# Kernel tuning notes

Hardware: AMD Instinct MI355X
Metric: run time of the kernel (lower is better)

## Reference

```python
import jax, jax.numpy as jnp
import numpy as np
import math

B, T, C = 2, 2048, 2048
NH = 16
HS = C // NH            # 128
N_ELEM = int(0.5 * HS)  # 64, rotary_percentage=0.5
A_T = 10                # adapter_prompt_length


def setup_inputs() -> dict:
    key = jax.random.key(0)
    ks = jax.random.split(key, 8)
    x = jax.random.normal(ks[0], (B, T, C), dtype=jnp.float32)
    # RoPE cache: standard cos/sin of shape (T, n_elem)
    theta = 10000.0 ** (-jnp.arange(0, N_ELEM, 2, dtype=jnp.float32) / N_ELEM)
    pos = jnp.arange(T, dtype=jnp.float32)
    ang = pos[:, None] * theta[None, :]           # (T, n_elem/2)
    ang = jnp.concatenate([ang, ang], axis=-1)    # (T, n_elem)
    cos, sin = jnp.cos(ang), jnp.sin(ang)
    mask = jnp.tril(jnp.ones((T, T), dtype=bool))  # causal
    s = 0.02
    attn_w = jax.random.normal(ks[1], (3 * C, C), dtype=jnp.float32) * s
    attn_b = jax.random.normal(ks[2], (3 * C,), dtype=jnp.float32) * s
    proj_w = jax.random.normal(ks[3], (C, C), dtype=jnp.float32) * s
    proj_b = jax.random.normal(ks[4], (C,), dtype=jnp.float32) * s
    adapter_wte = jax.random.normal(ks[5], (A_T, C), dtype=jnp.float32) * s
    gating_factor = jnp.full((1,), 0.1, dtype=jnp.float32)  # nonzero so adapter path matters
    return {"x": x, "cos": cos, "sin": sin, "mask": mask,
            "attn_w": attn_w, "attn_b": attn_b, "proj_w": proj_w, "proj_b": proj_b,
            "adapter_wte": adapter_wte, "gating_factor": gating_factor}


def apply_rope(t, cos, sin):
    # t: (B, nh, T, n_elem); cos/sin: (T, n_elem)
    half = t.shape[-1] // 2
    t1, t2 = t[..., :half], t[..., half:]
    rotated = jnp.concatenate([-t2, t1], axis=-1)
    return t * cos + rotated * sin


def sdpa(q, k, v, mask, scale):
    # q: (B,nh,Tq,hs), k/v: (B,nh,Tk,hs); mask: bool broadcastable to (Tq,Tk) or None
    s = jnp.einsum('bhqd,bhkd->bhqk', q, k) * scale
    if mask is not None:
        s = jnp.where(mask, s, jnp.finfo(s.dtype).min)
    p = jax.nn.softmax(s, axis=-1)
    return jnp.einsum('bhqk,bhkd->bhqd', p, v)


def reference(x, cos, sin, mask, attn_w, attn_b, proj_w, proj_b, adapter_wte, gating_factor):
    scale = 1.0 / math.sqrt(HS)
    qkv = x @ attn_w.T + attn_b                    # (B,T,3C)
    qkv = qkv.reshape(B, T, NH, 3 * HS).transpose(0, 2, 1, 3)  # (B,nh,T,3hs)
    q, k, v = jnp.split(qkv, 3, axis=-1)           # each (B,nh,T,hs)
    q = jnp.concatenate([apply_rope(q[..., :N_ELEM], cos, sin), q[..., N_ELEM:]], axis=-1)
    k = jnp.concatenate([apply_rope(k[..., :N_ELEM], cos, sin), k[..., N_ELEM:]], axis=-1)
    y = sdpa(q, k, v, mask, scale)                 # (B,nh,T,hs)
    # adapter-prefix attention
    a_qkv = adapter_wte @ attn_w.T + attn_b        # (aT, 3C)
    _, ak, av = jnp.split(a_qkv, 3, axis=-1)       # (aT, C) each
    ak = ak.reshape(1, A_T, NH, HS).transpose(0, 2, 1, 3)  # (1,nh,aT,hs)
    av = av.reshape(1, A_T, NH, HS).transpose(0, 2, 1, 3)
    ak = jnp.broadcast_to(ak, (B, NH, A_T, HS))
    av = jnp.broadcast_to(av, (B, NH, A_T, HS))
    ay = sdpa(q, ak, av, None, scale)              # full (no mask)
    y = y + gating_factor * ay
    y = y.transpose(0, 2, 1, 3).reshape(B, T, C)
    return y @ proj_w.T + proj_b
```

## Files before the change

### kernel.cpp

```cpp
#include <hip/hip_runtime.h>
#include <math.h>

#define B_DIM 2
#define T_DIM 2048
#define C_DIM 2048
#define NHEAD 16
#define HS 128
#define QKV_N 6144
#define AT 10
#define M_DIM 4096

using bf16x8 = __attribute__((ext_vector_type(8))) short;
using f32x4v = __attribute__((ext_vector_type(4))) float;

__device__ __forceinline__ unsigned short f2bf(float f) {
    union { float f; unsigned int u; } cv; cv.f = f;
    unsigned int u = cv.u;
    return (unsigned short)((u + 0x7FFFu + ((u >> 16) & 1u)) >> 16);
}
__device__ __forceinline__ float bf2f(unsigned short h) {
    union { unsigned int u; float f; } cv; cv.u = ((unsigned int)h) << 16;
    return cv.f;
}
__device__ __forceinline__ unsigned int pack_bf16(float lo, float hi) {
    unsigned int r;
    asm volatile("v_cvt_pk_bf16_f32 %0, %1, %2" : "=v"(r) : "v"(lo), "v"(hi));
    return r;
}
__device__ __forceinline__ void gload_lds16(const void* g, void* l) {
    __builtin_amdgcn_global_load_lds(
        (const __attribute__((address_space(1))) void*)g,
        (__attribute__((address_space(3))) void*)l, 16, 0, 0);
}

__global__ __launch_bounds__(256)
void f32_to_bf16_kernel(const float* __restrict__ in, unsigned short* __restrict__ out, int n8) {
    const int i = blockIdx.x * 256 + threadIdx.x;
    if (i >= n8) return;
    const float4 a = *(const float4*)&in[(size_t)i * 8];
    const float4 b = *(const float4*)&in[(size_t)i * 8 + 4];
    *(ushort4*)&out[(size_t)i * 8]     = make_ushort4(f2bf(a.x), f2bf(a.y), f2bf(a.z), f2bf(a.w));
    *(ushort4*)&out[(size_t)i * 8 + 4] = make_ushort4(f2bf(b.x), f2bf(b.y), f2bf(b.z), f2bf(b.w));
}

template<int FUSED>
__global__ __launch_bounds__(256)
void gemm_pipe(const unsigned short* __restrict__ A, const unsigned short* __restrict__ Bw,
               const float* __restrict__ bias, float* __restrict__ Cf32,
               const float* __restrict__ cosb, const float* __restrict__ sinb,
               unsigned short* __restrict__ Qb, unsigned short* __restrict__ Kb,
               unsigned short* __restrict__ Vt, int M, int N, int K) {
    __shared__ unsigned short As[3][4096];
    __shared__ unsigned short Bs[3][4096];

    const int tid  = threadIdx.x;
    const int wave = tid >> 6;
    const int lane = tid & 63;

    const int ncnt = gridDim.x, mcnt = gridDim.y;
    const int nwg = ncnt * mcnt;
    int bid = blockIdx.y * ncnt + blockIdx.x;
    bid = (bid & 7) * (nwg >> 3) + (bid >> 3);
    const int mt = (bid >> 3) % mcnt;
    const int nt = (bid / (mcnt * 8)) * 8 + (bid & 7);
    const int m0 = mt * 128, n0 = nt * 128;

    const int wr = (wave >> 1) * 64;
    const int wc = (wave & 1) * 64;
    const int fr = lane & 15;
    const int hi = lane >> 4;

    const int srow = lane >> 2;
    const int sk   = 8 * ((lane & 3) ^ ((lane >> 3) & 3));
    const int swk  = 8 * (hi ^ ((fr >> 1) & 3));

    auto STAGE = [&](int ks, int bi) {
        const int k0 = ks << 5;
#pragma unroll
        for (int t = 0; t < 2; ++t) {
            const int seg = wave * 2 + t;
            gload_lds16(&A[(size_t)(m0 + seg * 16 + srow) * K + k0 + sk], &As[bi][seg * 512]);
            gload_lds16(&Bw[(size_t)(n0 + seg * 16 + srow) * K + k0 + sk], &Bs[bi][seg * 512]);
        }
    };

    f32x4v acc[4][4];
#pragma unroll
    for (int i = 0; i < 4; ++i)
#pragma unroll
        for (int j = 0; j < 4; ++j)
#pragma unroll
            for (int q = 0; q < 4; ++q) acc[i][j][q] = 0.f;

    const int nk = K >> 5;
    STAGE(0, 0);
    STAGE(1, 1);

    for (int ks = 0; ks < nk; ++ks) {
        if (ks < nk - 1) asm volatile("s_waitcnt vmcnt(4)" ::: "memory");
        else             asm volatile("s_waitcnt vmcnt(0)" ::: "memory");
        __builtin_amdgcn_sched_barrier(0);
        __builtin_amdgcn_s_barrier();
        asm volatile("" ::: "memory");
        __builtin_amdgcn_sched_barrier(0);

        const unsigned short* Ab = As[ks % 3];
        const unsigned short* Bb = Bs[ks % 3];
        bf16x8 af[4], bfg[4];
#pragma unroll
        for (int i = 0; i < 4; ++i)
            af[i] = *(const bf16x8*)&Ab[(wr + i * 16 + fr) * 32 + swk];
#pragma unroll
        for (int j = 0; j < 4; ++j)
            bfg[j] = *(const bf16x8*)&Bb[(wc + j * 16 + fr) * 32 + swk];

        if (ks + 2 < nk) STAGE(ks + 2, (ks + 2) % 3);

        __builtin_amdgcn_s_setprio(1);
#pragma unroll
        for (int i = 0; i < 4; ++i)
#pragma unroll
            for (int j = 0; j < 4; ++j)
                acc[i][j] = __builtin_amdgcn_mfma_f32_16x16x32_bf16(af[i], bfg[j], acc[i][j], 0, 0, 0);
        __builtin_amdgcn_s_setprio(0);
    }

    const int r4 = hi * 4;
    if constexpr (FUSED) {
        const int part = (n0 >> 7) % 3;
        const int head = n0 / 384;
        const int bh   = (m0 >> 11) * NHEAD + head;
        if (part == 2) {
#pragma unroll
            for (int i = 0; i < 4; ++i) {
                const int t0v = (m0 & (T_DIM - 1)) + wr + i * 16 + r4;
#pragma unroll
                for (int j = 0; j < 4; ++j) {
                    const int d = wc + j * 16 + fr;
                    const float bv = bias[n0 + d];
                    ushort4 o = make_ushort4(f2bf(acc[i][j][0] + bv), f2bf(acc[i][j][1] + bv),
                                             f2bf(acc[i][j][2] + bv), f2bf(acc[i][j][3] + bv));
                    *(ushort4*)&Vt[((size_t)bh * HS + d) * T_DIM + t0v] = o;
                }
            }
        } else {
            unsigned short* Dst = part ? Kb : Qb;
            if (wc == 0) {
#pragma unroll
                for (int i = 0; i < 4; ++i) {
#pragma unroll
                    for (int q = 0; q < 4; ++q) {
                        const int t = (m0 & (T_DIM - 1)) + wr + i * 16 + r4 + q;
                        const float* crow = &cosb[t * 64];
                        const float* srw  = &sinb[t * 64];
                        unsigned short* drow = &Dst[((size_t)bh * T_DIM + t) * HS];
#pragma unroll
                        for (int j = 0; j < 2; ++j) {
                            const int d = j * 16 + fr;
                            const float v1 = acc[i][j][q]     + bias[n0 + d];
                            const float v2 = acc[i][j + 2][q] + bias[n0 + d + 32];
                            drow[d]      = f2bf(v1 * crow[d]      - v2 * srw[d]);
                            drow[d + 32] = f2bf(v2 * crow[d + 32] + v1 * srw[d + 32]);
                        }
                    }
                }
            } else {
#pragma unroll
                for (int i = 0; i < 4; ++i) {
                    const int t0r = (m0 & (T_DIM - 1)) + wr + i * 16 + r4;
#pragma unroll
                    for (int j = 0; j < 4; ++j) {
                        const int d = 64 + j * 16 + fr;
                        const float bv = bias[n0 + d];
                        unsigned short* dcol = &Dst[((size_t)bh * T_DIM + t0r) * HS + d];
#pragma unroll
                        for (int q = 0; q < 4; ++q)
                            dcol[(size_t)q * HS] = f2bf(acc[i][j][q] + bv);
                    }
                }
            }
        }
    } else {
#pragma unroll
        for (int i = 0; i < 4; ++i) {
#pragma unroll
            for (int j = 0; j < 4; ++j) {
                const int col = n0 + wc + j * 16 + fr;
                const float bv = bias[col];
#pragma unroll
                for (int q = 0; q < 4; ++q) {
                    const int row = m0 + wr + i * 16 + r4 + q;
                    Cf32[(size_t)row * N + col] = acc[i][j][q] + bv;
                }
            }
        }
    }
}

__global__ __launch_bounds__(64)
void adapter_qkv_kernel(const float* __restrict__ wte, const unsigned short* __restrict__ wb,
                        const float* __restrict__ bias, float* __restrict__ aqkv) {
    const int n = blockIdx.x;
    const int lane = threadIdx.x;
    float acc[AT];
#pragma unroll
    for (int a = 0; a < AT; ++a) acc[a] = 0.f;
    for (int k = lane * 8; k < C_DIM; k += 64 * 8) {
        const ushort4 wa = *(const ushort4*)&wb[(size_t)n * C_DIM + k];
        const ushort4 wc = *(const ushort4*)&wb[(size_t)n * C_DIM + k + 4];
        const float w0 = bf2f(wa.x), w1 = bf2f(wa.y), w2 = bf2f(wa.z), w3 = bf2f(wa.w);
        const float w4 = bf2f(wc.x), w5 = bf2f(wc.y), w6 = bf2f(wc.z), w7 = bf2f(wc.w);
#pragma unroll
        for (int a = 0; a < AT; ++a) {
            const float4 t0 = *(const float4*)&wte[(size_t)a * C_DIM + k];
            const float4 t1 = *(const float4*)&wte[(size_t)a * C_DIM + k + 4];
            acc[a] += w0 * t0.x + w1 * t0.y + w2 * t0.z + w3 * t0.w
                    + w4 * t1.x + w5 * t1.y + w6 * t1.z + w7 * t1.w;
        }
    }
#pragma unroll
    for (int a = 0; a < AT; ++a) {
        float v = acc[a];
        for (int off = 32; off; off >>= 1) v += __shfl_down(v, off);
        if (lane == 0) aqkv[(size_t)a * QKV_N + n] = v + bias[n];
    }
}

__global__ __launch_bounds__(256)
void flash_mfma(const unsigned short* __restrict__ Qb, const unsigned short* __restrict__ Kb,
                const unsigned short* __restrict__ Vt, const float* __restrict__ aqkv,
                const float* __restrict__ gating, unsigned short* __restrict__ yb) {
    __shared__ __align__(16) unsigned short smem[2][16384];

    const int tid = threadIdx.x;
    const int wave = tid >> 6, lane = tid & 63;
    const int lo = lane & 15, hi = lane >> 4;

    const int z = blockIdx.x & 15;
    const int h = (blockIdx.x >> 4) & 15;
    const int b = blockIdx.x >> 8;
    const int bh = b * NHEAD + h;
    const float kscale = 0.08838834764831845f * 1.4426950408889634f;

    const unsigned short* Qh = Qb + (size_t)bh * T_DIM * HS;
    const unsigned short* Kh = Kb + (size_t)bh * T_DIM * HS;
    const unsigned short* Vh = Vt + (size_t)bh * HS * T_DIM;

    float* AK = (float*)&smem[0][0];
    float* AV = AK + AT * HS;

    auto STAGE = [&](int k0, int bufi) {
        unsigned short* Kd = &smem[bufi][0];
        unsigned short* Vd = &smem[bufi][8192];
#pragma unroll
        for (int t = 0; t < 4; ++t) {
            const int kr = wave * 16 + t * 4 + hi;
            gload_lds16(Kh + (size_t)(k0 + kr) * HS + 8 * (lo ^ (kr & 7)),
                        &Kd[(wave * 16 + t * 4) * 128]);
            const int vr = (wave * 4 + t) * 8 + (lane >> 3);
            gload_lds16(Vh + (size_t)vr * T_DIM + k0 + 8 * ((lane & 7) ^ (vr & 7)),
                        &Vd[(wave * 4 + t) * 8 * 64]);
        }
    };

#pragma unroll 1
    for (int pass = 0; pass < 2; ++pass) {
        const int qt = pass ? z : (31 - z);
        const int q0 = qt * 64;
        const int myqrow = q0 + wave * 16 + lo;

        bf16x8 qf[4];
        {
            const unsigned short* qrow = Qh + (size_t)myqrow * HS;
#pragma unroll
            for (int c = 0; c < 4; ++c) qf[c] = *(const bf16x8*)&qrow[c * 32 + hi * 8];
        }

        f32x4v oacc[8];
#pragma unroll
        for (int d = 0; d < 8; ++d)
#pragma unroll
            for (int q = 0; q < 4; ++q) oacc[d][q] = 0.f;
        float m = -INFINITY, ln = 0.f;

        STAGE(0, 0);
        int cur = 0;
        for (int kt = 0; kt <= qt; ++kt) {
            const int k0 = kt * 64;
            __syncthreads();
            if (kt < qt) STAGE(k0 + 64, cur ^ 1);
            const unsigned short* Ks = &smem[cur][0];
            const unsigned short* Vs = &smem[cur][8192];

            f32x4v sacc[4];
            __builtin_amdgcn_s_setprio(1);
#pragma unroll
            for (int s = 0; s < 4; ++s) {
#pragma unroll
                for (int q = 0; q < 4; ++q) sacc[s][q] = 0.f;
                const int krow = s * 16 + lo;
                const int rs = (lo & 7) << 4;
#pragma unroll
                for (int c = 0; c < 4; ++c) {
                    const int boff = (c * 64 + hi * 16) ^ rs;
                    bf16x8 kf = *(const bf16x8*)&Ks[krow * 128 + (boff >> 1)];
                    sacc[s] = __builtin_amdgcn_mfma_f32_16x16x32_bf16(kf, qf[c], sacc[s], 0, 0, 0);
                }
            }
            __builtin_amdgcn_s_setprio(0);

            const bool dtile = (kt == qt);
            float p[4][4];
            float xm = -INFINITY;
#pragma unroll
            for (int s = 0; s < 4; ++s)
#pragma unroll
                for (int q = 0; q < 4; ++q) {
                    float v = sacc[s][q] * kscale;
                    if (dtile && (k0 + s * 16 + hi * 4 + q > myqrow)) v = -INFINITY;
                    p[s][q] = v;
                    xm = fmaxf(xm, v);
                }
            xm = fmaxf(xm, __shfl_xor(xm, 16));
            xm = fmaxf(xm, __shfl_xor(xm, 32));
            if (__any(xm > m + 11.5f)) {
                const float mnew = fmaxf(m, xm);
                const float al = exp2f(m - mnew);
                m = mnew;
                ln *= al;
                float aq[4];
#pragma unroll
                for (int q = 0; q < 4; ++q) aq[q] = __shfl(al, hi * 4 + q);
#pragma unroll
                for (int d = 0; d < 8; ++d)
#pragma unroll
                    for (int q = 0; q < 4; ++q) oacc[d][q] *= aq[q];
            }
            float psum = 0.f;
#pragma unroll
            for (int s = 0; s < 4; ++s)
#pragma unroll
                for (int q = 0; q < 4; ++q) {
                    p[s][q] = exp2f(p[s][q] - m);
                    psum += p[s][q];
                }
            psum += __shfl_xor(psum, 16);
            psum += __shfl_xor(psum, 32);
            ln += psum;

            unsigned int pk[4][2];
#pragma unroll
            for (int s = 0; s < 4; ++s) {
                pk[s][0] = pack_bf16(p[s][0], p[s][1]);
                pk[s][1] = pack_bf16(p[s][2], p[s][3]);
            }
            const int src0 = lo + ((hi & 1) << 5);
            const int src1 = src0 + 16;
            const bool shi = (hi >> 1) != 0;
#pragma unroll
            for (int c = 0; c < 2; ++c) {
                const unsigned int a0 = (unsigned int)__shfl((int)pk[c*2][0], src0);
                const unsigned int b0 = (unsigned int)__shfl((int)pk[c*2+1][0], src0);
                const unsigned int a1 = (unsigned int)__shfl((int)pk[c*2][1], src0);
                const unsigned int b1 = (unsigned int)__shfl((int)pk[c*2+1][1], src0);
                const unsigned int a2 = (unsigned int)__shfl((int)pk[c*2][0], src1);
                const unsigned int b2 = (unsigned int)__shfl((int)pk[c*2+1][0], src1);
                const unsigned int a3 = (unsigned int)__shfl((int)pk[c*2][1], src1);
                const unsigned int b3 = (unsigned int)__shfl((int)pk[c*2+1][1], src1);
                union { unsigned int u[4]; bf16x8 v; } cv2;
                cv2.u[0] = shi ? b0 : a0;
                cv2.u[1] = shi ? b1 : a1;
                cv2.u[2] = shi ? b2 : a2;
                cv2.u[3] = shi ? b3 : a3;
                const bf16x8 pf = cv2.v;
                __builtin_amdgcn_s_setprio(1);
#pragma unroll
                for (int d = 0; d < 8; ++d) {
                    const int vrow = d * 16 + lo;
                    const int boff = (c * 64 + hi * 16) ^ ((lo & 7) << 4);
                    bf16x8 vf = *(const bf16x8*)&Vs[vrow * 64 + (boff >> 1)];
                    oacc[d] = __builtin_amdgcn_mfma_f32_16x16x32_bf16(pf, vf, oacc[d], 0, 0, 0);
                }
                __builtin_amdgcn_s_setprio(0);
            }
            cur ^= 1;
        }

        float linv[4];
#pragma unroll
        for (int q = 0; q < 4; ++q) linv[q] = 1.f / __shfl(ln, hi * 4 + q);
#pragma unroll
        for (int d = 0; d < 8; ++d)
#pragma unroll
            for (int q = 0; q < 4; ++q) oacc[d][q] *= linv[q];

        __syncthreads();
        for (int idx = tid; idx < AT * HS; idx += 256) {
            const int a = idx >> 7, d = idx & 127;
            AK[idx] = aqkv[(size_t)a * QKV_N + C_DIM + h * HS + d];
            AV[idx] = aqkv[(size_t)a * QKV_N + 2 * C_DIM + h * HS + d];
        }
        __syncthreads();

        float qflt[4][8];
#pragma unroll
        for (int c = 0; c < 4; ++c)
#pragma unroll
            for (int j = 0; j < 8; ++j) qflt[c][j] = bf2f((unsigned short)qf[c][j]);

        float e[AT];
        float amax = -INFINITY;
#pragma unroll
        for (int a = 0; a < AT; ++a) {
            float t = 0.f;
#pragma unroll
            for (int c = 0; c < 4; ++c) {
                const float4 k0v = *(const float4*)&AK[a * HS + c * 32 + hi * 8];
                const float4 k1v = *(const float4*)&AK[a * HS + c * 32 + hi * 8 + 4];
                t += qflt[c][0] * k0v.x + qflt[c][1] * k0v.y + qflt[c][2] * k0v.z + qflt[c][3] * k0v.w
                   + qflt[c][4] * k1v.x + qflt[c][5] * k1v.y + qflt[c][6] * k1v.z + qflt[c][7] * k1v.w;
            }
            t += __shfl_xor(t, 16);
            t += __shfl_xor(t, 32);
            e[a] = t * 0.08838834764831845f;
            amax = fmaxf(amax, e[a]);
        }
        float asum = 0.f;
#pragma unroll
        for (int a = 0; a < AT; ++a) { e[a] = __expf(e[a] - amax); asum += e[a]; }
        const float gcoef = gating[0] / asum;

#pragma unroll
        for (int a = 0; a < AT; ++a) {
            const float ca = e[a] * gcoef;
            float cq[4];
#pragma unroll
            for (int q = 0; q < 4; ++q) cq[q] = __shfl(ca, hi * 4 + q);
#pragma unroll
            for (int d = 0; d < 8; ++d) {
                const float av = AV[a * HS + d * 16 + lo];
#pragma unroll
                for (int q = 0; q < 4; ++q) oacc[d][q] += cq[q] * av;
            }
        }

#pragma unroll
        for (int q = 0; q < 4; ++q) {
            const int row = q0 + wave * 16 + hi * 4 + q;
            unsigned short* dst = yb + ((size_t)(b * T_DIM + row)) * C_DIM + h * HS + lo;
#pragma unroll
            for (int d = 0; d < 8; ++d) dst[d * 16] = f2bf(oacc[d][q]);
        }

        if (pass == 0) __syncthreads();
    }
}

extern "C" void kernel_launch(void* const* d_in, const int* in_sizes, int n_in,
                              void* d_out, int out_size, void* d_ws, size_t ws_size,
                              hipStream_t stream) {
    const float* x       = (const float*)d_in[0];
    const float* cosb    = (const float*)d_in[1];
    const float* sinb    = (const float*)d_in[2];
    const float* attn_w  = (const float*)d_in[4];
    const float* attn_b  = (const float*)d_in[5];
    const float* proj_w  = (const float*)d_in[6];
    const float* proj_b  = (const float*)d_in[7];
    const float* wte     = (const float*)d_in[8];
    const float* gating  = (const float*)d_in[9];
    float* out = (float*)d_out;

    float* aqkv = (float*)d_ws;
    unsigned short* xb  = (unsigned short*)(aqkv + (size_t)AT * QKV_N);
    unsigned short* awb = xb  + (size_t)M_DIM * C_DIM;
    unsigned short* Qb  = awb + (size_t)QKV_N * C_DIM;
    unsigned short* Kb  = Qb  + (size_t)B_DIM * NHEAD * T_DIM * HS;
    unsigned short* Vt  = Kb  + (size_t)B_DIM * NHEAD * T_DIM * HS;
    unsigned short* pwb = Vt  + (size_t)B_DIM * NHEAD * T_DIM * HS;
    unsigned short* yv  = pwb + (size_t)C_DIM * C_DIM;

    f32_to_bf16_kernel<<<(M_DIM * C_DIM / 8 + 255) / 256, 256, 0, stream>>>(x, xb, M_DIM * C_DIM / 8);
    f32_to_bf16_kernel<<<(QKV_N * C_DIM / 8 + 255) / 256, 256, 0, stream>>>(attn_w, awb, QKV_N * C_DIM / 8);
    gemm_pipe<1><<<dim3(QKV_N / 128, M_DIM / 128), 256, 0, stream>>>(
        xb, awb, attn_b, nullptr, cosb, sinb, Qb, Kb, Vt, M_DIM, QKV_N, C_DIM);
    adapter_qkv_kernel<<<QKV_N, 64, 0, stream>>>(wte, awb, attn_b, aqkv);
    f32_to_bf16_kernel<<<(C_DIM * C_DIM / 8 + 255) / 256, 256, 0, stream>>>(proj_w, pwb, C_DIM * C_DIM / 8);
    flash_mfma<<<B_DIM * NHEAD * 16, 256, 0, stream>>>(Qb, Kb, Vt, aqkv, gating, yv);
    gemm_pipe<0><<<dim3(C_DIM / 128, M_DIM / 128), 256, 0, stream>>>(
        yv, pwb, proj_b, out, nullptr, nullptr, nullptr, nullptr, nullptr, M_DIM, C_DIM, C_DIM);
}
```

Measured before the change: 437.1 us.

## Use 256x256 tiles with 512 threads for fused QKV GEMM

```diff
diff --git a/kernel.cpp b/kernel.cpp
--- a/kernel.cpp
+++ b/kernel.cpp
@@ -43,13 +43,152 @@
     *(ushort4*)&out[(size_t)i * 8 + 4] = make_ushort4(f2bf(b.x), f2bf(b.y), f2bf(b.z), f2bf(b.w));
 }
 
-template<int FUSED>
+__global__ __launch_bounds__(512)
+void gemm_qkv256(const unsigned short* __restrict__ A, const unsigned short* __restrict__ Bw,
+                 const float* __restrict__ bias,
+                 const float* __restrict__ cosb, const float* __restrict__ sinb,
+                 unsigned short* __restrict__ Qb, unsigned short* __restrict__ Kb,
+                 unsigned short* __restrict__ Vt, int M, int N, int K) {
+    __shared__ unsigned short As[3][8192];
+    __shared__ unsigned short Bs[3][8192];
+
+    const int tid  = threadIdx.x;
+    const int wave = tid >> 6;
+    const int lane = tid & 63;
+
+    const int ncnt = gridDim.x, mcnt = gridDim.y;
+    const int nwg = ncnt * mcnt;
+    int bid = blockIdx.y * ncnt + blockIdx.x;
+    bid = (bid & 7) * (nwg >> 3) + (bid >> 3);
+    const int mt = (bid >> 3) % mcnt;
+    const int nt = (bid / (mcnt * 8)) * 8 + (bid & 7);
+    const int m0 = mt * 256, n0 = nt * 256;
+
+    const int wr   = (wave >> 2) * 128;
+    const int wcol = (wave & 3) * 64;
+    const int fr = lane & 15;
+    const int hi = lane >> 4;
+
+    const int srow = lane >> 2;
+    const int sk   = 8 * ((lane & 3) ^ ((lane >> 3) & 3));
+    const int swk  = 8 * (hi ^ ((fr >> 1) & 3));
+
+    auto STAGE = [&](int ks, int bi) {
+        const int k0 = ks << 5;
+#pragma unroll
+        for (int t = 0; t < 2; ++t) {
+            const int seg = wave * 2 + t;
+            gload_lds16(&A[(size_t)(m0 + seg * 16 + srow) * K + k0 + sk], &As[bi][seg * 512]);
+            gload_lds16(&Bw[(size_t)(n0 + seg * 16 + srow) * K + k0 + sk], &Bs[bi][seg * 512]);
+        }
+    };
+
+    f32x4v acc[8][4];
+#pragma unroll
+    for (int i = 0; i < 8; ++i)
+#pragma unroll
+        for (int j = 0; j < 4; ++j)
+#pragma unroll
+            for (int q = 0; q < 4; ++q) acc[i][j][q] = 0.f;
+
+    const int nk = K >> 5;
+    STAGE(0, 0);
+    STAGE(1, 1);
+
+    for (int ks = 0; ks < nk; ++ks) {
+        if (ks < nk - 1) asm volatile("s_waitcnt vmcnt(4)" ::: "memory");
+        else             asm volatile("s_waitcnt vmcnt(0)" ::: "memory");
+        __builtin_amdgcn_sched_barrier(0);
+        __builtin_amdgcn_s_barrier();
+        asm volatile("" ::: "memory");
+        __builtin_amdgcn_sched_barrier(0);
+
+        const unsigned short* Ab = As[ks % 3];
+        const unsigned short* Bb = Bs[ks % 3];
+        bf16x8 af[8], bfg[4];
+#pragma unroll
+        for (int i = 0; i < 8; ++i)
+            af[i] = *(const bf16x8*)&Ab[(wr + i * 16 + fr) * 32 + swk];
+#pragma unroll
+        for (int j = 0; j < 4; ++j)
+            bfg[j] = *(const bf16x8*)&Bb[(wcol + j * 16 + fr) * 32 + swk];
+
+        if (ks + 2 < nk) STAGE(ks + 2, (ks + 2) % 3);
+
+        __builtin_amdgcn_s_setprio(1);
+#pragma unroll
+        for (int i = 0; i < 8; ++i)
+#pragma unroll
+            for (int j = 0; j < 4; ++j)
+                acc[i][j] = __builtin_amdgcn_mfma_f32_16x16x32_bf16(af[i], bfg[j], acc[i][j], 0, 0, 0);
+        __builtin_amdgcn_s_setprio(0);
+    }
+
+    const int r4   = hi * 4;
+    const int ncb  = n0 + wcol;
+    const int head = ncb / 384;
+    const int rem  = ncb % 384;
+    const int part = rem >> 7;
+    const int po   = rem & 127;
+    const int bh   = (m0 >> 11) * NHEAD + head;
+    const int tbase = (m0 & (T_DIM - 1)) + wr;
+
+    if (part == 2) {
+#pragma unroll
+        for (int i = 0; i < 8; ++i) {
+            const int t0v = tbase + i * 16 + r4;
+#pragma unroll
+            for (int j = 0; j < 4; ++j) {
+                const int d = po + j * 16 + fr;
+                const float bv = bias[ncb + j * 16 + fr];
+                ushort4 o = make_ushort4(f2bf(acc[i][j][0] + bv), f2bf(acc[i][j][1] + bv),
+                                         f2bf(acc[i][j][2] + bv), f2bf(acc[i][j][3] + bv));
+                *(ushort4*)&Vt[((size_t)bh * HS + d) * T_DIM + t0v] = o;
+            }
+        }
+    } else {
+        unsigned short* Dst = part ? Kb : Qb;
+        if (po == 0) {
+#pragma unroll
+            for (int i = 0; i < 8; ++i) {
+#pragma unroll
+                for (int q = 0; q < 4; ++q) {
+                    const int t = tbase + i * 16 + r4 + q;
+                    const float* crow = &cosb[t * 64];
+                    const float* srw  = &sinb[t * 64];
+                    unsigned short* drow = &Dst[((size_t)bh * T_DIM + t) * HS];
+#pragma unroll
+                    for (int j = 0; j < 2; ++j) {
+                        const int d = j * 16 + fr;
+                        const float v1 = acc[i][j][q]     + bias[ncb + d];
+                        const float v2 = acc[i][j + 2][q] + bias[ncb + d + 32];
+                        drow[d]      = f2bf(v1 * crow[d]      - v2 * srw[d]);
+                        drow[d + 32] = f2bf(v2 * crow[d + 32] + v1 * srw[d + 32]);
+                    }
+                }
+            }
+        } else {
+#pragma unroll
+            for (int i = 0; i < 8; ++i) {
+                const int t0r = tbase + i * 16 + r4;
+#pragma unroll
+                for (int j = 0; j < 4; ++j) {
+                    const int d = 64 + j * 16 + fr;
+                    const float bv = bias[ncb + j * 16 + fr];
+                    unsigned short* dcol = &Dst[((size_t)bh * T_DIM + t0r) * HS + d];
+#pragma unroll
+                    for (int q = 0; q < 4; ++q)
+                        dcol[(size_t)q * HS] = f2bf(acc[i][j][q] + bv);
+                }
+            }
+        }
+    }
+}
+
 __global__ __launch_bounds__(256)
 void gemm_pipe(const unsigned short* __restrict__ A, const unsigned short* __restrict__ Bw,
                const float* __restrict__ bias, float* __restrict__ Cf32,
-               const float* __restrict__ cosb, const float* __restrict__ sinb,
-               unsigned short* __restrict__ Qb, unsigned short* __restrict__ Kb,
-               unsigned short* __restrict__ Vt, int M, int N, int K) {
+               int M, int N, int K) {
     __shared__ unsigned short As[3][4096];
     __shared__ unsigned short Bs[3][4096];
 
@@ -126,72 +265,16 @@
     }
 
     const int r4 = hi * 4;
-    if constexpr (FUSED) {
-        const int part = (n0 >> 7) % 3;
-        const int head = n0 / 384;
-        const int bh   = (m0 >> 11) * NHEAD + head;
-        if (part == 2) {
-#pragma unroll
-            for (int i = 0; i < 4; ++i) {
-                const int t0v = (m0 & (T_DIM - 1)) + wr + i * 16 + r4;
-#pragma unroll
-                for (int j = 0; j < 4; ++j) {
-                    const int d = wc + j * 16 + fr;
-                    const float bv = bias[n0 + d];
-                    ushort4 o = make_ushort4(f2bf(acc[i][j][0] + bv), f2bf(acc[i][j][1] + bv),
-                                             f2bf(acc[i][j][2] + bv), f2bf(acc[i][j][3] + bv));
-                    *(ushort4*)&Vt[((size_t)bh * HS + d) * T_DIM + t0v] = o;
-                }
-            }
-        } else {
-            unsigned short* Dst = part ? Kb : Qb;
-            if (wc == 0) {
-#pragma unroll
-                for (int i = 0; i < 4; ++i) {
-#pragma unroll
-                    for (int q = 0; q < 4; ++q) {
-                        const int t = (m0 & (T_DIM - 1)) + wr + i * 16 + r4 + q;
-                        const float* crow = &cosb[t * 64];
-                        const float* srw  = &sinb[t * 64];
-                        unsigned short* drow = &Dst[((size_t)bh * T_DIM + t) * HS];
-#pragma unroll
-                        for (int j = 0; j < 2; ++j) {
-                            const int d = j * 16 + fr;
-                            const float v1 = acc[i][j][q]     + bias[n0 + d];
-                            const float v2 = acc[i][j + 2][q] + bias[n0 + d + 32];
-                            drow[d]      = f2bf(v1 * crow[d]      - v2 * srw[d]);
-                            drow[d + 32] = f2bf(v2 * crow[d + 32] + v1 * srw[d + 32]);
-                        }
-                    }
-                }
-            } else {
-#pragma unroll
-                for (int i = 0; i < 4; ++i) {
-                    const int t0r = (m0 & (T_DIM - 1)) + wr + i * 16 + r4;
-#pragma unroll
-                    for (int j = 0; j < 4; ++j) {
-                        const int d = 64 + j * 16 + fr;
-                        const float bv = bias[n0 + d];
-                        unsigned short* dcol = &Dst[((size_t)bh * T_DIM + t0r) * HS + d];
-#pragma unroll
-                        for (int q = 0; q < 4; ++q)
-                            dcol[(size_t)q * HS] = f2bf(acc[i][j][q] + bv);
-                    }
-                }
-            }
-        }
-    } else {
-#pragma unroll
-        for (int i = 0; i < 4; ++i) {
-#pragma unroll
-            for (int j = 0; j < 4; ++j) {
-                const int col = n0 + wc + j * 16 + fr;
-                const float bv = bias[col];
-#pragma unroll
-                for (int q = 0; q < 4; ++q) {
-                    const int row = m0 + wr + i * 16 + r4 + q;
-                    Cf32[(size_t)row * N + col] = acc[i][j][q] + bv;
-                }
+#pragma unroll
+    for (int i = 0; i < 4; ++i) {
+#pragma unroll
+        for (int j = 0; j < 4; ++j) {
+            const int col = n0 + wc + j * 16 + fr;
+            const float bv = bias[col];
+#pragma unroll
+            for (int q = 0; q < 4; ++q) {
+                const int row = m0 + wr + i * 16 + r4 + q;
+                Cf32[(size_t)row * N + col] = acc[i][j][q] + bv;
             }
         }
     }
@@ -481,11 +564,11 @@
 
     f32_to_bf16_kernel<<<(M_DIM * C_DIM / 8 + 255) / 256, 256, 0, stream>>>(x, xb, M_DIM * C_DIM / 8);
     f32_to_bf16_kernel<<<(QKV_N * C_DIM / 8 + 255) / 256, 256, 0, stream>>>(attn_w, awb, QKV_N * C_DIM / 8);
-    gemm_pipe<1><<<dim3(QKV_N / 128, M_DIM / 128), 256, 0, stream>>>(
-        xb, awb, attn_b, nullptr, cosb, sinb, Qb, Kb, Vt, M_DIM, QKV_N, C_DIM);
+    gemm_qkv256<<<dim3(QKV_N / 256, M_DIM / 256), 512, 0, stream>>>(
+        xb, awb, attn_b, cosb, sinb, Qb, Kb, Vt, M_DIM, QKV_N, C_DIM);
     adapter_qkv_kernel<<<QKV_N, 64, 0, stream>>>(wte, awb, attn_b, aqkv);
     f32_to_bf16_kernel<<<(C_DIM * C_DIM / 8 + 255) / 256, 256, 0, stream>>>(proj_w, pwb, C_DIM * C_DIM / 8);
     flash_mfma<<<B_DIM * NHEAD * 16, 256, 0, stream>>>(Qb, Kb, Vt, aqkv, gating, yv);
-    gemm_pipe<0><<<dim3(C_DIM / 128, M_DIM / 128), 256, 0, stream>>>(
-        yv, pwb, proj_b, out, nullptr, nullptr, nullptr, nullptr, nullptr, M_DIM, C_DIM, C_DIM);
-}
+    gemm_pipe<<<dim3(C_DIM / 128, M_DIM / 128), 256, 0, stream>>>(
+        yv, pwb, proj_b, out, M_DIM, C_DIM, C_DIM);
+}
```

After: 442.5 us. No clear change (+1.2%).
